# Optimization experiments

Measured on AMD Instinct MI355X. Metric: run time of the kernel, lower is better.

The kernel has to match this reference:

```python
import jax, jax.numpy as jnp
from jax import lax
import numpy as np

B, T, C, H = 1024, 256, 6, 32  # batch, time, channels (6 LSTMs), hidden
G = 4 * H  # gate dim (i,f,g,o), PyTorch order


def setup_inputs() -> dict:
    key = jax.random.key(0)
    ks = jax.random.split(key, 12)
    s = 1.0 / np.sqrt(H)  # PyTorch LSTM/Linear init scale
    u = lambda k, shape, sc: jax.random.uniform(k, shape, jnp.float32, -sc, sc)
    x = jax.random.normal(ks[0], (B, T, C), jnp.float32)
    # 6 channel-wise LSTMs stacked on leading axis (input_size=1 -> w_ih is [C, G])
    w_ih = u(ks[1], (C, G), s)
    w_hh = u(ks[2], (C, G, H), s)
    b_ih = u(ks[3], (C, G), s)
    b_hh = u(ks[4], (C, G), s)
    # MLP head: fc1 (192->64), fc3 (64->64), fc2 (64->2), PyTorch Linear layout [out,in]
    s1 = 1.0 / np.sqrt(C * H)
    w1 = u(ks[5], (64, C * H), s1); b1 = u(ks[6], (64,), s1)
    s3 = 1.0 / np.sqrt(64)
    w3 = u(ks[7], (64, 64), s3); b3 = u(ks[8], (64,), s3)
    w2 = u(ks[9], (2, 64), s3); b2 = u(ks[10], (2,), s3)
    return {"x": x, "w_ih": w_ih, "w_hh": w_hh, "b_ih": b_ih, "b_hh": b_hh,
            "w1": w1, "b1": b1, "w3": w3, "b3": b3, "w2": w2, "b2": b2}


def _grouped_lstm(x, w_ih, w_hh, b_ih, b_hh):
    # x: [B, T, C]; runs C independent hidden-32 LSTMs fused in one scan.
    b = b_ih + b_hh  # [C, G]

    def step(carry, x_t):
        h, c = carry  # [B, C, H] each
        gates = x_t[:, :, None] * w_ih[None] + jnp.einsum('cgh,bch->bcg', w_hh, h) + b
        i, f, g, o = jnp.split(gates, 4, axis=-1)
        c = jax.nn.sigmoid(f) * c + jax.nn.sigmoid(i) * jnp.tanh(g)
        h = jax.nn.sigmoid(o) * jnp.tanh(c)
        return (h, c), h

    h0 = jnp.zeros((x.shape[0], C, H), x.dtype)
    _, hs = lax.scan(step, (h0, h0), jnp.swapaxes(x, 0, 1))  # hs: [T, B, C, H]
    return jnp.transpose(hs, (1, 0, 2, 3)).reshape(x.shape[0], x.shape[1], C * H)


def reference(x, w_ih, w_hh, b_ih, b_hh, w1, b1, w3, b3, w2, b2):
    x7 = _grouped_lstm(x, w_ih, w_hh, b_ih, b_hh)  # [B, T, 192] == cat of 6 LSTM outputs
    h = jax.nn.relu(x7[:, -1, :] @ w1.T + b1)
    h = jax.nn.relu(h @ w3.T + b3)
    out = h @ w2.T + b2  # [B, 2]
    return (out, x7)
```

## Files before the change

### kernel.cpp

```cpp
#include <hip/hip_runtime.h>
#include <hip/hip_bf16.h>


#define Bv 1024
#define Tv 256
#define Cv 6
#define Hv 32
#define Gv 128

#define L2E 1.442695041f

typedef _Float16 f16x8 __attribute__((ext_vector_type(8)));
typedef float f32x4v __attribute__((ext_vector_type(4)));

__device__ __forceinline__ float fsig(float v) {
    return __builtin_amdgcn_rcpf(1.0f + __builtin_amdgcn_exp2f(v * -L2E));
}
__device__ __forceinline__ float ftanh2(float v) {
    float u = __builtin_amdgcn_rcpf(1.0f + __builtin_amdgcn_exp2f(v * (-2.0f * L2E)));
    return fmaf(u, 2.0f, -1.0f);
}

__global__ __launch_bounds__(128) void lstm_kernel(
    const float* __restrict__ x,
    const float* __restrict__ w_ih,
    const float* __restrict__ w_hh,
    const float* __restrict__ b_ih,
    const float* __restrict__ b_hh,
    float* __restrict__ x7)
{
    __shared__ _Float16 hlds[2][16][40];

    const int tid  = threadIdx.x;
    const int wv   = tid >> 6;
    const int lane = tid & 63;
    const int r16  = lane & 15;
    const int grp  = lane >> 4;

    const int c  = blockIdx.x % Cv;
    const int nb = (blockIdx.x / Cv) * 16;

    {
        _Float16* hz = &hlds[0][0][0];
        for (int i = tid; i < 2 * 16 * 40; i += 128) hz[i] = (_Float16)0.0f;
    }

    const float* whc = w_hh + (size_t)c * (Gv * Hv);
    f16x8 afrag[4];
    #pragma unroll
    for (int q = 0; q < 4; ++q) {
        const float* wr = whc + (q * 32 + wv * 16 + r16) * Hv + grp * 8;
        float4 wa = *(const float4*)(wr);
        float4 wb = *(const float4*)(wr + 4);
        f16x8 a;
        a[0] = (_Float16)wa.x; a[1] = (_Float16)wa.y;
        a[2] = (_Float16)wa.z; a[3] = (_Float16)wa.w;
        a[4] = (_Float16)wb.x; a[5] = (_Float16)wb.y;
        a[6] = (_Float16)wb.z; a[7] = (_Float16)wb.w;
        afrag[q] = a;
    }
    float4 bias4[4], wih4[4];
    #pragma unroll
    for (int q = 0; q < 4; ++q) {
        const int rb = q * 32 + wv * 16 + grp * 4;
        float4 bi = *(const float4*)(b_ih + c * Gv + rb);
        float4 bh = *(const float4*)(b_hh + c * Gv + rb);
        bias4[q] = make_float4(bi.x + bh.x, bi.y + bh.y, bi.z + bh.z, bi.w + bh.w);
        wih4[q]  = *(const float4*)(w_ih + c * Gv + rb);
    }

    float cst[4] = {0.0f, 0.0f, 0.0f, 0.0f};
    const float* xp = x + ((size_t)(nb + r16) * Tv) * Cv + c;
    float* op = x7 + ((size_t)(nb + r16) * Tv) * (Cv * Hv) + c * Hv + wv * 16 + grp * 4;

    __syncthreads();

    float xt = xp[0];
    int p = 0;
    for (int t = 0; t < Tv; ++t) {
        int tn = (t + 1 < Tv) ? (t + 1) : (Tv - 1);
        float xn = xp[tn * Cv];

        f16x8 bfrag = *(const f16x8*)(&hlds[p][r16][grp * 8]);

        f32x4v acc[4];
        #pragma unroll
        for (int q = 0; q < 4; ++q) {
            acc[q][0] = fmaf(xt, wih4[q].x, bias4[q].x);
            acc[q][1] = fmaf(xt, wih4[q].y, bias4[q].y);
            acc[q][2] = fmaf(xt, wih4[q].z, bias4[q].z);
            acc[q][3] = fmaf(xt, wih4[q].w, bias4[q].w);
            acc[q] = __builtin_amdgcn_mfma_f32_16x16x32_f16(afrag[q], bfrag, acc[q], 0, 0, 0);
        }

        float h4[4];
        #pragma unroll
        for (int r = 0; r < 4; ++r) {
            float i_s = fsig(acc[0][r]);
            float f_s = fsig(acc[1][r]);
            float g_t = ftanh2(acc[2][r]);
            float o_s = fsig(acc[3][r]);
            float cr  = fmaf(f_s, cst[r], i_s * g_t);
            cst[r] = cr;
            h4[r] = o_s * ftanh2(cr);
        }

        *(float4*)(op + (size_t)t * (Cv * Hv)) = make_float4(h4[0], h4[1], h4[2], h4[3]);

        auto pk0 = __builtin_amdgcn_cvt_pkrtz(h4[0], h4[1]);
        auto pk1 = __builtin_amdgcn_cvt_pkrtz(h4[2], h4[3]);
        uint2 pk = make_uint2(__builtin_bit_cast(unsigned int, pk0),
                              __builtin_bit_cast(unsigned int, pk1));
        *(uint2*)(&hlds[p ^ 1][r16][wv * 16 + grp * 4]) = pk;

        __syncthreads();
        p ^= 1;
        xt = xn;
    }
}

__global__ __launch_bounds__(64) void head_kernel(
    const float* __restrict__ x7,
    const float* __restrict__ w1, const float* __restrict__ b1,
    const float* __restrict__ w3, const float* __restrict__ b3,
    const float* __restrict__ w2, const float* __restrict__ b2,
    float* __restrict__ out)
{
    const int b   = blockIdx.x;
    const int tid = threadIdx.x;
    __shared__ float xr[Cv * Hv];
    __shared__ float h1[64];
    __shared__ float h2s[64];

    const float* xrow = x7 + ((size_t)b * Tv + (Tv - 1)) * (Cv * Hv);
    if (tid < 48) ((float4*)xr)[tid] = ((const float4*)xrow)[tid];
    __syncthreads();

    float acc[4] = {0.f, 0.f, 0.f, 0.f};
    const float4* w4 = (const float4*)(w1 + tid * (Cv * Hv));
    const float4* x4 = (const float4*)xr;
    #pragma unroll
    for (int k = 0; k < 48; ++k) {
        float4 w = w4[k], xv = x4[k];
        acc[k & 3] += (w.x * xv.x + w.y * xv.y) + (w.z * xv.z + w.w * xv.w);
    }
    h1[tid] = fmaxf((acc[0] + acc[1]) + (acc[2] + acc[3]) + b1[tid], 0.0f);
    __syncthreads();

    float bcc[4] = {0.f, 0.f, 0.f, 0.f};
    const float4* w34 = (const float4*)(w3 + tid * 64);
    const float4* h14 = (const float4*)h1;
    #pragma unroll
    for (int k = 0; k < 16; ++k) {
        float4 w = w34[k], hv = h14[k];
        bcc[k & 3] += (w.x * hv.x + w.y * hv.y) + (w.z * hv.z + w.w * hv.w);
    }
    h2s[tid] = fmaxf((bcc[0] + bcc[1]) + (bcc[2] + bcc[3]) + b3[tid], 0.0f);
    __syncthreads();

    if (tid < 2) {
        float a2 = b2[tid];
        const float* w2r = w2 + tid * 64;
        #pragma unroll 4
        for (int k = 0; k < 64; ++k) a2 += w2r[k] * h2s[k];
        out[b * 2 + tid] = a2;
    }
}

extern "C" void kernel_launch(void* const* d_in, const int* in_sizes, int n_in,
                              void* d_out, int out_size, void* d_ws, size_t ws_size,
                              hipStream_t stream) {
    const float* x    = (const float*)d_in[0];
    const float* w_ih = (const float*)d_in[1];
    const float* w_hh = (const float*)d_in[2];
    const float* b_ih = (const float*)d_in[3];
    const float* b_hh = (const float*)d_in[4];
    const float* w1   = (const float*)d_in[5];
    const float* b1   = (const float*)d_in[6];
    const float* w3   = (const float*)d_in[7];
    const float* b3   = (const float*)d_in[8];
    const float* w2   = (const float*)d_in[9];
    const float* b2   = (const float*)d_in[10];

    float* out = (float*)d_out;
    float* x7  = out + (size_t)Bv * 2;

    lstm_kernel<<<dim3((Bv / 16) * Cv), dim3(128), 0, stream>>>(x, w_ih, w_hh, b_ih, b_hh, x7);
    head_kernel<<<dim3(Bv), dim3(64), 0, stream>>>(x7, w1, b1, w3, b3, w2, b2, out);
}
```

Baseline: 395.4 us.

## Run each LSTM tile in a single wavefront and drop per-step barriers

Shrinks each block from two wavefronts to one, so a single wave computes all 128 gate rows for 16 batch rows with 8 MFMAs per step. Because one wave owns the whole hidden-state tile, the LDS double buffer and the per-timestep __syncthreads are removed, relying on in-order LDS access within a wave. The cost is that each wave now does twice the MFMA and activation work serially on the recurrence's critical path, with less parallelism per block and more registers per thread.

```diff
diff --git a/kernel.cpp b/kernel.cpp
--- a/kernel.cpp
+++ b/kernel.cpp
@@ -21,7 +21,7 @@
     return fmaf(u, 2.0f, -1.0f);
 }
 
-__global__ __launch_bounds__(128) void lstm_kernel(
+__global__ __launch_bounds__(64) void lstm_kernel(
     const float* __restrict__ x,
     const float* __restrict__ w_ih,
     const float* __restrict__ w_hh,
@@ -29,27 +29,22 @@
     const float* __restrict__ b_hh,
     float* __restrict__ x7)
 {
-    __shared__ _Float16 hlds[2][16][40];
+    __shared__ _Float16 hlds[16][40];
 
-    const int tid  = threadIdx.x;
-    const int wv   = tid >> 6;
-    const int lane = tid & 63;
+    const int lane = threadIdx.x;
     const int r16  = lane & 15;
     const int grp  = lane >> 4;
 
     const int c  = blockIdx.x % Cv;
     const int nb = (blockIdx.x / Cv) * 16;
 
-    {
-        _Float16* hz = &hlds[0][0][0];
-        for (int i = tid; i < 2 * 16 * 40; i += 128) hz[i] = (_Float16)0.0f;
-    }
+    for (int i = lane; i < 16 * 40; i += 64) (&hlds[0][0])[i] = (_Float16)0.0f;
 
     const float* whc = w_hh + (size_t)c * (Gv * Hv);
-    f16x8 afrag[4];
+    f16x8 afrag[8];
     #pragma unroll
-    for (int q = 0; q < 4; ++q) {
-        const float* wr = whc + (q * 32 + wv * 16 + r16) * Hv + grp * 8;
+    for (int q = 0; q < 8; ++q) {
+        const float* wr = whc + (q * 16 + r16) * Hv + grp * 8;
         float4 wa = *(const float4*)(wr);
         float4 wb = *(const float4*)(wr + 4);
         f16x8 a;
@@ -59,33 +54,31 @@
         a[6] = (_Float16)wb.z; a[7] = (_Float16)wb.w;
         afrag[q] = a;
     }
-    float4 bias4[4], wih4[4];
+    float4 bias4[8], wih4[8];
     #pragma unroll
-    for (int q = 0; q < 4; ++q) {
-        const int rb = q * 32 + wv * 16 + grp * 4;
+    for (int q = 0; q < 8; ++q) {
+        const int rb = q * 16 + grp * 4;
         float4 bi = *(const float4*)(b_ih + c * Gv + rb);
         float4 bh = *(const float4*)(b_hh + c * Gv + rb);
         bias4[q] = make_float4(bi.x + bh.x, bi.y + bh.y, bi.z + bh.z, bi.w + bh.w);
         wih4[q]  = *(const float4*)(w_ih + c * Gv + rb);
     }
 
-    float cst[4] = {0.0f, 0.0f, 0.0f, 0.0f};
+    float cst[8] = {0.f, 0.f, 0.f, 0.f, 0.f, 0.f, 0.f, 0.f};
+
     const float* xp = x + ((size_t)(nb + r16) * Tv) * Cv + c;
-    float* op = x7 + ((size_t)(nb + r16) * Tv) * (Cv * Hv) + c * Hv + wv * 16 + grp * 4;
-
-    __syncthreads();
+    float* op = x7 + ((size_t)(nb + r16) * Tv) * (Cv * Hv) + c * Hv + grp * 4;
 
     float xt = xp[0];
-    int p = 0;
     for (int t = 0; t < Tv; ++t) {
         int tn = (t + 1 < Tv) ? (t + 1) : (Tv - 1);
         float xn = xp[tn * Cv];
 
-        f16x8 bfrag = *(const f16x8*)(&hlds[p][r16][grp * 8]);
+        f16x8 bfrag = *(const f16x8*)(&hlds[r16][grp * 8]);
 
-        f32x4v acc[4];
+        f32x4v acc[8];
         #pragma unroll
-        for (int q = 0; q < 4; ++q) {
+        for (int q = 0; q < 8; ++q) {
             acc[q][0] = fmaf(xt, wih4[q].x, bias4[q].x);
             acc[q][1] = fmaf(xt, wih4[q].y, bias4[q].y);
             acc[q][2] = fmaf(xt, wih4[q].z, bias4[q].z);
@@ -93,28 +86,37 @@
             acc[q] = __builtin_amdgcn_mfma_f32_16x16x32_f16(afrag[q], bfrag, acc[q], 0, 0, 0);
         }
 
-        float h4[4];
+        float hv[8];
         #pragma unroll
-        for (int r = 0; r < 4; ++r) {
-            float i_s = fsig(acc[0][r]);
-            float f_s = fsig(acc[1][r]);
-            float g_t = ftanh2(acc[2][r]);
-            float o_s = fsig(acc[3][r]);
-            float cr  = fmaf(f_s, cst[r], i_s * g_t);
-            cst[r] = cr;
-            h4[r] = o_s * ftanh2(cr);
+        for (int q2 = 0; q2 < 2; ++q2) {
+            #pragma unroll
+            for (int r = 0; r < 4; ++r) {
+                const int u = q2 * 4 + r;
+                float i_s = fsig(acc[q2][r]);
+                float f_s = fsig(acc[q2 + 2][r]);
+                float g_t = ftanh2(acc[q2 + 4][r]);
+                float o_s = fsig(acc[q2 + 6][r]);
+                float cr  = fmaf(f_s, cst[u], i_s * g_t);
+                cst[u] = cr;
+                hv[u] = o_s * ftanh2(cr);
+            }
         }
 
-        *(float4*)(op + (size_t)t * (Cv * Hv)) = make_float4(h4[0], h4[1], h4[2], h4[3]);
+        float* ot = op + (size_t)t * (Cv * Hv);
+        *(float4*)(ot)      = make_float4(hv[0], hv[1], hv[2], hv[3]);
+        *(float4*)(ot + 16) = make_float4(hv[4], hv[5], hv[6], hv[7]);
 
-        auto pk0 = __builtin_amdgcn_cvt_pkrtz(h4[0], h4[1]);
-        auto pk1 = __builtin_amdgcn_cvt_pkrtz(h4[2], h4[3]);
-        uint2 pk = make_uint2(__builtin_bit_cast(unsigned int, pk0),
-                              __builtin_bit_cast(unsigned int, pk1));
-        *(uint2*)(&hlds[p ^ 1][r16][wv * 16 + grp * 4]) = pk;
+        auto pk0 = __builtin_amdgcn_cvt_pkrtz(hv[0], hv[1]);
+        auto pk1 = __builtin_amdgcn_cvt_pkrtz(hv[2], hv[3]);
+        auto pk2 = __builtin_amdgcn_cvt_pkrtz(hv[4], hv[5]);
+        auto pk3 = __builtin_amdgcn_cvt_pkrtz(hv[6], hv[7]);
+        *(uint2*)(&hlds[r16][grp * 4]) =
+            make_uint2(__builtin_bit_cast(unsigned int, pk0),
+                       __builtin_bit_cast(unsigned int, pk1));
+        *(uint2*)(&hlds[r16][16 + grp * 4]) =
+            make_uint2(__builtin_bit_cast(unsigned int, pk2),
+                       __builtin_bit_cast(unsigned int, pk3));
 
-        __syncthreads();
-        p ^= 1;
         xt = xn;
     }
 }
@@ -185,6 +187,6 @@
     float* out = (float*)d_out;
     float* x7  = out + (size_t)Bv * 2;
 
-    lstm_kernel<<<dim3((Bv / 16) * Cv), dim3(128), 0, stream>>>(x, w_ih, w_hh, b_ih, b_hh, x7);
+    lstm_kernel<<<dim3((Bv / 16) * Cv), dim3(64), 0, stream>>>(x, w_ih, w_hh, b_ih, b_hh, x7);
     head_kernel<<<dim3(Bv), dim3(64), 0, stream>>>(x7, w1, b1, w3, b3, w2, b2, out);
 }
```

New measurement: 393.2 us. No clear change (-0.5%).
